# Kernel tuning notes

Measured on AMD Instinct MI355X. Metric: run time of the kernel, lower is better.

Reference implementation:

```python
import jax, jax.numpy as jnp
import numpy as np

B, T, D, U = 32, 512, 256, 1024

def setup_inputs() -> dict:
    key = jax.random.key(0)
    ks = jax.random.split(key, 5)
    return {
        "X_vecs": jax.random.normal(ks[0], (B, D), dtype=jnp.float32),
        "X_ts": jax.random.normal(ks[1], (B, T, D), dtype=jnp.float32),
        "mat_A_0": jax.random.normal(ks[2], (D, U), dtype=jnp.float32) * (1.0 / np.sqrt(D)),
        "vec_b_0": jnp.zeros((1, U), dtype=jnp.float32),
        "mat_A_s": jax.random.normal(ks[3], (D, U), dtype=jnp.float32) * (1.0 / np.sqrt(D)),
        "vec_b_s": jnp.zeros((1, U), dtype=jnp.float32),
        "mat_W_d": jax.random.normal(ks[4], (D, U), dtype=jnp.float32) * (1.0 / np.sqrt(D)),
        "vec_b_d": jnp.zeros((1, U), dtype=jnp.float32),
    }

def reference(X_vecs, X_ts, mat_A_0, vec_b_0, mat_A_s, vec_b_s, mat_W_d, vec_b_d):
    softsign = jax.nn.soft_sign  # x / (1 + |x|), the layer's main_activation
    # Learned initial state: H_0 = softsign(X_vecs @ A_0 + b_0)   [B, U]
    H0 = softsign(X_vecs @ mat_A_0 + vec_b_0)
    # Static per-step drive from the vector input (computed once, reused each t)
    drive = X_vecs @ mat_A_s + vec_b_s + vec_b_d  # [B, U]
    # Batched projection of the whole timeseries (one big GEMM instead of T small ones)
    XW = jnp.einsum('btd,du->btu', X_ts, mat_W_d)  # [B, T, U]
    def step(h, x_t):  # h: [B,U], x_t: [B,U]
        h_new = softsign(h + drive + x_t)
        return h_new, h_new
    _, outs = jax.lax.scan(step, H0, jnp.swapaxes(XW, 0, 1))  # outs: [T, B, U]
    return jnp.swapaxes(outs, 0, 1)  # return_sequences=True -> [B, T, U]
```

## Files before the change

kernel.cpp:

```cpp
#include <hip/hip_runtime.h>

#define B_DIM 32
#define T_DIM 512
#define D_DIM 256
#define U_DIM 1024
#define M_DIM (B_DIM * T_DIM)

typedef __bf16 bf16_t;
typedef bf16_t bf16x8 __attribute__((ext_vector_type(8)));
typedef float f32x4 __attribute__((ext_vector_type(4)));

__device__ __forceinline__ float ssign(float z) {
    return z * __builtin_amdgcn_rcpf(1.0f + __builtin_fabsf(z));
}

__global__ __launch_bounds__(256) void prep(const float* __restrict__ Wd,
                                            bf16_t* __restrict__ Wt,
                                            const float* __restrict__ X,
                                            bf16_t* __restrict__ Xb,
                                            const float* __restrict__ Xv,
                                            const float* __restrict__ A0,
                                            const float* __restrict__ b0,
                                            const float* __restrict__ As,
                                            const float* __restrict__ bs,
                                            const float* __restrict__ bd,
                                            float* __restrict__ H0o,
                                            float* __restrict__ Dro) {
    const int bid = blockIdx.x;
    if (bid < 64) {
        __shared__ float tile[64][65];
        const int tx = threadIdx.x & 63;
        const int ty = threadIdx.x >> 6;
        const int n0 = (bid & 15) * 64;
        const int k0 = (bid >> 4) * 64;
        #pragma unroll
        for (int rr = 0; rr < 16; ++rr) {
            const int kk = ty * 16 + rr;
            tile[kk][tx] = Wd[(size_t)(k0 + kk) * U_DIM + n0 + tx];
        }
        __syncthreads();
        #pragma unroll
        for (int rr = 0; rr < 16; ++rr) {
            const int nn = ty * 16 + rr;
            Wt[(size_t)(n0 + nn) * D_DIM + k0 + tx] = (bf16_t)tile[tx][nn];
        }
    } else if (bid < 2112) {
        const int i = ((bid - 64) * 256 + threadIdx.x) * 8;
        const float4 a = *(const float4*)(X + i);
        const float4 b = *(const float4*)(X + i + 4);
        bf16x8 p;
        p[0]=(bf16_t)a.x; p[1]=(bf16_t)a.y; p[2]=(bf16_t)a.z; p[3]=(bf16_t)a.w;
        p[4]=(bf16_t)b.x; p[5]=(bf16_t)b.y; p[6]=(bf16_t)b.z; p[7]=(bf16_t)b.w;
        *(bf16x8*)(Xb + i) = p;
    } else {
        __shared__ float xv[D_DIM];
        const int idx = bid - 2112;
        const int b = idx >> 2;
        const int u = (idx & 3) * 256 + threadIdx.x;
        xv[threadIdx.x] = Xv[(size_t)b * D_DIM + threadIdx.x];
        __syncthreads();
        float a0 = 0.f, asum = 0.f;
        #pragma unroll 8
        for (int d = 0; d < D_DIM; ++d) {
            const float x = xv[d];
            a0   = fmaf(x, A0[(size_t)d * U_DIM + u], a0);
            asum = fmaf(x, As[(size_t)d * U_DIM + u], asum);
        }
        H0o[(size_t)b * U_DIM + u] = ssign(a0 + b0[u]);
        Dro[(size_t)b * U_DIM + u] = asum + bs[u] + bd[u];
    }
}

__global__ __launch_bounds__(128, 1) void fused3(
        const float* __restrict__ H0w, const float* __restrict__ Drw,
        const bf16_t* __restrict__ Xb, const bf16_t* __restrict__ Wt,
        float* __restrict__ out) {
    __shared__ float xwT[4][64 * 20];

    const int lane = threadIdx.x & 63;
    const int wid = threadIdx.x >> 6;
    const int b = blockIdx.x;
    const int u0 = blockIdx.y * 64;

#define BARX()                                                          \
    do {                                                                \
        __asm__ volatile("s_waitcnt lgkmcnt(0)" ::: "memory");          \
        __builtin_amdgcn_s_barrier();                                   \
        __asm__ volatile("" ::: "memory");                              \
    } while (0)

    if (wid == 1) {
        const int lm = lane & 15, q = lane >> 4;
        const bf16_t* xrow = Xb + ((size_t)b * T_DIM + lm) * D_DIM + q * 8;

#define LOADA(DST, CH)                                                              \
    {                                                                               \
        const bf16_t* xp_ = xrow + (size_t)(CH) * 16 * D_DIM;                       \
        _Pragma("unroll")                                                           \
        for (int kb = 0; kb < 8; ++kb) DST[kb] = *(const bf16x8*)(xp_ + kb * 32);   \
    }

        bf16x8 af0[8], af1[8], af2[8], af3[8];
        LOADA(af0, 0); LOADA(af1, 1); LOADA(af2, 2); LOADA(af3, 3);

        bf16x8 bW[4][8];
        #pragma unroll
        for (int n = 0; n < 4; ++n)
            #pragma unroll
            for (int kb = 0; kb < 8; ++kb)
                bW[n][kb] = *(const bf16x8*)(Wt + (size_t)(u0 + n * 16 + lm) * D_DIM + kb * 32 + q * 8);

        f32x4 acc[4];
#define ZACC()                                                                      \
    {                                                                               \
        _Pragma("unroll")                                                           \
        for (int n = 0; n < 4; ++n) acc[n] = (f32x4){0.f, 0.f, 0.f, 0.f};           \
    }
#define MM(AF)                                                                      \
    {                                                                               \
        _Pragma("unroll")                                                           \
        for (int kb = 0; kb < 8; ++kb) {                                            \
            _Pragma("unroll")                                                       \
            for (int n = 0; n < 4; ++n)                                             \
                acc[n] = __builtin_amdgcn_mfma_f32_16x16x32_bf16(AF[kb], bW[n][kb], \
                                                                 acc[n], 0, 0, 0);  \
        }                                                                           \
    }
#define STASHS(SLOT)                                                                \
    {                                                                               \
        _Pragma("unroll")                                                           \
        for (int n = 0; n < 4; ++n)                                                 \
            *(f32x4*)&xwT[SLOT][(n * 16 + lm) * 20 + q * 4] = acc[n];               \
    }

        ZACC(); MM(af0); STASHS(0);
        ZACC(); MM(af1); STASHS(1);
        BARX();

        #pragma unroll 1
        for (int cc = 0; cc < 32; cc += 4) {
            if (cc + 2 < 32) { if (cc + 4 < 32) LOADA(af0, cc + 4);
                               ZACC(); MM(af2); STASHS(2); }
            BARX();
            if (cc + 3 < 32) { if (cc + 5 < 32) LOADA(af1, cc + 5);
                               ZACC(); MM(af3); STASHS(3); }
            BARX();
            if (cc + 4 < 32) { if (cc + 6 < 32) LOADA(af2, cc + 6);
                               ZACC(); MM(af0); STASHS(0); }
            BARX();
            if (cc + 5 < 32) { if (cc + 7 < 32) LOADA(af3, cc + 7);
                               ZACC(); MM(af1); STASHS(1); }
            BARX();
        }
#undef LOADA
#undef ZACC
#undef MM
#undef STASHS
    } else {
        const int u = u0 + lane;
        float h = H0w[(size_t)b * U_DIM + u];
        const float drive = Drw[(size_t)b * U_DIM + u];
        float* po = out + (size_t)b * T_DIM * U_DIM + u;

        BARX();
        const float* rb0 = &xwT[0][lane * 20];
        f32x4 v0 = *(const f32x4*)(rb0 + 0);
        f32x4 v1 = *(const f32x4*)(rb0 + 4);
        f32x4 v2 = *(const f32x4*)(rb0 + 8);
        f32x4 v3 = *(const f32x4*)(rb0 + 12);

        #pragma unroll 1
        for (int c = 0; c < 32; ++c) {
            const float* rbn = &xwT[(c + 1) & 3][lane * 20];
            f32x4 n0 = *(const f32x4*)(rbn + 0);
            f32x4 n1 = *(const f32x4*)(rbn + 4);
            f32x4 n2 = *(const f32x4*)(rbn + 8);
            f32x4 n3 = *(const f32x4*)(rbn + 12);

            float dv[16];
            #pragma unroll
            for (int r = 0; r < 4; ++r) {
                dv[r]      = drive + v0[r];
                dv[4 + r]  = drive + v1[r];
                dv[8 + r]  = drive + v2[r];
                dv[12 + r] = drive + v3[r];
            }
            #pragma unroll
            for (int j = 0; j < 16; ++j) {
                h = ssign(h + dv[j]);
                po[(size_t)(c * 16 + j) * U_DIM] = h;
            }
            BARX();
            v0 = n0; v1 = n1; v2 = n2; v3 = n3;
        }
    }
#undef BARX
}

__global__ __launch_bounds__(256) void gemm_xw_f32(const float* __restrict__ Xts,
                                                   const float* __restrict__ Wd,
                                                   float* __restrict__ out) {
    __shared__ float xs[16 * D_DIM];
    const int tid = threadIdx.x;
    const int bt0 = blockIdx.y * 16;
    const int u = blockIdx.x * 256 + tid;
    const float4* src4 = (const float4*)(Xts + (size_t)bt0 * D_DIM);
    float4* xs4 = (float4*)xs;
    #pragma unroll
    for (int i = 0; i < 4; ++i) xs4[tid + 256 * i] = src4[tid + 256 * i];
    __syncthreads();
    float acc[16];
    #pragma unroll
    for (int r = 0; r < 16; ++r) acc[r] = 0.0f;
    const float* wp = Wd + u;
    for (int d0 = 0; d0 < D_DIM; d0 += 4) {
        const float w0 = wp[(size_t)(d0 + 0) * U_DIM];
        const float w1 = wp[(size_t)(d0 + 1) * U_DIM];
        const float w2 = wp[(size_t)(d0 + 2) * U_DIM];
        const float w3 = wp[(size_t)(d0 + 3) * U_DIM];
        #pragma unroll
        for (int r = 0; r < 16; ++r) {
            const float4 xvv = *(const float4*)&xs[r * D_DIM + d0];
            acc[r] = fmaf(xvv.x, w0, acc[r]);
            acc[r] = fmaf(xvv.y, w1, acc[r]);
            acc[r] = fmaf(xvv.z, w2, acc[r]);
            acc[r] = fmaf(xvv.w, w3, acc[r]);
        }
    }
    #pragma unroll
    for (int r = 0; r < 16; ++r)
        out[(size_t)(bt0 + r) * U_DIM + u] = acc[r];
}

__global__ __launch_bounds__(256) void scan_old(const float* __restrict__ Xv,
                                                const float* __restrict__ A0,
                                                const float* __restrict__ b0,
                                                const float* __restrict__ As,
                                                const float* __restrict__ bs,
                                                const float* __restrict__ bd,
                                                float* __restrict__ out) {
    __shared__ float xv[D_DIM];
    const int tid = threadIdx.x;
    const int b = blockIdx.y;
    const int u = blockIdx.x * 256 + tid;
    xv[tid] = Xv[(size_t)b * D_DIM + tid];
    __syncthreads();
    float a0 = 0.0f, asum = 0.0f;
    #pragma unroll 4
    for (int d = 0; d < D_DIM; ++d) {
        const float x = xv[d];
        a0   = fmaf(x, A0[(size_t)d * U_DIM + u], a0);
        asum = fmaf(x, As[(size_t)d * U_DIM + u], asum);
    }
    a0 += b0[u];
    const float drive = asum + bs[u] + bd[u];
    float h = ssign(a0);
    float* po = out + (size_t)b * T_DIM * U_DIM + u;
    float buf[8];
    #pragma unroll
    for (int i = 0; i < 8; ++i) buf[i] = po[(size_t)i * U_DIM];
    for (int t = 0; t < T_DIM; t += 8) {
        #pragma unroll
        for (int i = 0; i < 8; ++i) {
            const float x = buf[i];
            const int tn = t + i + 8;
            if (tn < T_DIM) buf[i] = po[(size_t)tn * U_DIM];
            h = ssign(h + drive + x);
            po[(size_t)(t + i) * U_DIM] = h;
        }
    }
}

extern "C" void kernel_launch(void* const* d_in, const int* in_sizes, int n_in,
                              void* d_out, int out_size, void* d_ws, size_t ws_size,
                              hipStream_t stream) {
    const float* Xv  = (const float*)d_in[0];
    const float* Xts = (const float*)d_in[1];
    const float* A0  = (const float*)d_in[2];
    const float* b0  = (const float*)d_in[3];
    const float* As  = (const float*)d_in[4];
    const float* bs  = (const float*)d_in[5];
    const float* Wd  = (const float*)d_in[6];
    const float* bd  = (const float*)d_in[7];
    float* out = (float*)d_out;

    const size_t OFF_H0 = 512u << 10;
    const size_t OFF_DR = 640u << 10;
    const size_t OFF_XB = 1u << 20;
    const size_t NEED   = 16u << 20;

    if (ws_size >= NEED) {
        bf16_t* Wt = (bf16_t*)d_ws;
        float* H0w = (float*)((char*)d_ws + OFF_H0);
        float* Drw = (float*)((char*)d_ws + OFF_DR);
        bf16_t* Xb = (bf16_t*)((char*)d_ws + OFF_XB);
        prep<<<dim3(64 + M_DIM * D_DIM / (256 * 8) + 128), dim3(256), 0, stream>>>(
            Wd, Wt, Xts, Xb, Xv, A0, b0, As, bs, bd, H0w, Drw);
        fused3<<<dim3(B_DIM, U_DIM / 64), dim3(128), 0, stream>>>(H0w, Drw, Xb, Wt, out);
    } else {
        gemm_xw_f32<<<dim3(U_DIM / 256, M_DIM / 16), dim3(256), 0, stream>>>(Xts, Wd, out);
        scan_old<<<dim3(U_DIM / 256, B_DIM), dim3(256), 0, stream>>>(Xv, A0, b0, As, bs, bd, out);
    }
}
```

Baseline: 129.5 us.

## Fold prep kernel into fused scan kernel, converting inputs to bf16 in-register

Drops the separate prep launch that converted X_ts and W_d to bf16 in workspace and computed H0 and the drive vector. The fused kernel now loads fp32 X_ts directly, converts it to bf16 in registers with a two-deep prefetch, and builds W_d fragments with strided fp32 loads. The scan wave computes H0 and the drive itself. This removes one launch and the workspace round-trip, at the cost of reading twice the bytes for X_ts, every block redoing the W_d and A_0/A_s loads with uncoalesced strided access, and more register pressure.

```diff
diff --git a/kernel.cpp b/kernel.cpp
--- a/kernel.cpp
+++ b/kernel.cpp
@@ -4,7 +4,6 @@
 #define T_DIM 512
 #define D_DIM 256
 #define U_DIM 1024
-#define M_DIM (B_DIM * T_DIM)
 
 typedef __bf16 bf16_t;
 typedef bf16_t bf16x8 __attribute__((ext_vector_type(8)));
@@ -14,68 +13,14 @@
     return z * __builtin_amdgcn_rcpf(1.0f + __builtin_fabsf(z));
 }
 
-__global__ __launch_bounds__(256) void prep(const float* __restrict__ Wd,
-                                            bf16_t* __restrict__ Wt,
-                                            const float* __restrict__ X,
-                                            bf16_t* __restrict__ Xb,
-                                            const float* __restrict__ Xv,
-                                            const float* __restrict__ A0,
-                                            const float* __restrict__ b0,
-                                            const float* __restrict__ As,
-                                            const float* __restrict__ bs,
-                                            const float* __restrict__ bd,
-                                            float* __restrict__ H0o,
-                                            float* __restrict__ Dro) {
-    const int bid = blockIdx.x;
-    if (bid < 64) {
-        __shared__ float tile[64][65];
-        const int tx = threadIdx.x & 63;
-        const int ty = threadIdx.x >> 6;
-        const int n0 = (bid & 15) * 64;
-        const int k0 = (bid >> 4) * 64;
-        #pragma unroll
-        for (int rr = 0; rr < 16; ++rr) {
-            const int kk = ty * 16 + rr;
-            tile[kk][tx] = Wd[(size_t)(k0 + kk) * U_DIM + n0 + tx];
-        }
-        __syncthreads();
-        #pragma unroll
-        for (int rr = 0; rr < 16; ++rr) {
-            const int nn = ty * 16 + rr;
-            Wt[(size_t)(n0 + nn) * D_DIM + k0 + tx] = (bf16_t)tile[tx][nn];
-        }
-    } else if (bid < 2112) {
-        const int i = ((bid - 64) * 256 + threadIdx.x) * 8;
-        const float4 a = *(const float4*)(X + i);
-        const float4 b = *(const float4*)(X + i + 4);
-        bf16x8 p;
-        p[0]=(bf16_t)a.x; p[1]=(bf16_t)a.y; p[2]=(bf16_t)a.z; p[3]=(bf16_t)a.w;
-        p[4]=(bf16_t)b.x; p[5]=(bf16_t)b.y; p[6]=(bf16_t)b.z; p[7]=(bf16_t)b.w;
-        *(bf16x8*)(Xb + i) = p;
-    } else {
-        __shared__ float xv[D_DIM];
-        const int idx = bid - 2112;
-        const int b = idx >> 2;
-        const int u = (idx & 3) * 256 + threadIdx.x;
-        xv[threadIdx.x] = Xv[(size_t)b * D_DIM + threadIdx.x];
-        __syncthreads();
-        float a0 = 0.f, asum = 0.f;
-        #pragma unroll 8
-        for (int d = 0; d < D_DIM; ++d) {
-            const float x = xv[d];
-            a0   = fmaf(x, A0[(size_t)d * U_DIM + u], a0);
-            asum = fmaf(x, As[(size_t)d * U_DIM + u], asum);
-        }
-        H0o[(size_t)b * U_DIM + u] = ssign(a0 + b0[u]);
-        Dro[(size_t)b * U_DIM + u] = asum + bs[u] + bd[u];
-    }
-}
-
-__global__ __launch_bounds__(128, 1) void fused3(
-        const float* __restrict__ H0w, const float* __restrict__ Drw,
-        const bf16_t* __restrict__ Xb, const bf16_t* __restrict__ Wt,
+__global__ __launch_bounds__(128, 1) void fusedall(
+        const float* __restrict__ Xv, const float* __restrict__ Xts,
+        const float* __restrict__ A0, const float* __restrict__ b0,
+        const float* __restrict__ As, const float* __restrict__ bs,
+        const float* __restrict__ Wd, const float* __restrict__ bd,
         float* __restrict__ out) {
     __shared__ float xwT[4][64 * 20];
+    __shared__ float xvs[D_DIM];
 
     const int lane = threadIdx.x & 63;
     const int wid = threadIdx.x >> 6;
@@ -91,24 +36,51 @@
 
     if (wid == 1) {
         const int lm = lane & 15, q = lane >> 4;
-        const bf16_t* xrow = Xb + ((size_t)b * T_DIM + lm) * D_DIM + q * 8;
-
-#define LOADA(DST, CH)                                                              \
-    {                                                                               \
-        const bf16_t* xp_ = xrow + (size_t)(CH) * 16 * D_DIM;                       \
-        _Pragma("unroll")                                                           \
-        for (int kb = 0; kb < 8; ++kb) DST[kb] = *(const bf16x8*)(xp_ + kb * 32);   \
-    }
-
-        bf16x8 af0[8], af1[8], af2[8], af3[8];
-        LOADA(af0, 0); LOADA(af1, 1); LOADA(af2, 2); LOADA(af3, 3);
+        const float* xrowf = Xts + ((size_t)b * T_DIM + lm) * D_DIM + q * 8;
+
+#define LOADF(FF, CH)                                                               \
+    {                                                                               \
+        const float* xp_ = xrowf + (size_t)(CH) * 16 * D_DIM;                       \
+        _Pragma("unroll")                                                           \
+        for (int t4 = 0; t4 < 16; ++t4)                                             \
+            FF[t4] = *(const f32x4*)(xp_ + (t4 >> 1) * 32 + (t4 & 1) * 4);          \
+    }
+#define CVT(AF, FF)                                                                 \
+    {                                                                               \
+        _Pragma("unroll")                                                           \
+        for (int kb = 0; kb < 8; ++kb) {                                            \
+            bf16x8 t_;                                                              \
+            _Pragma("unroll")                                                       \
+            for (int j = 0; j < 4; ++j) {                                           \
+                t_[j]     = (bf16_t)FF[kb * 2][j];                                  \
+                t_[4 + j] = (bf16_t)FF[kb * 2 + 1][j];                              \
+            }                                                                       \
+            AF[kb] = t_;                                                            \
+        }                                                                           \
+    }
+
+        f32x4 ff0[16], ff1[16];
+        LOADF(ff0, 0);
+        LOADF(ff1, 1);
 
         bf16x8 bW[4][8];
         #pragma unroll
-        for (int n = 0; n < 4; ++n)
+        for (int n = 0; n < 4; ++n) {
             #pragma unroll
-            for (int kb = 0; kb < 8; ++kb)
-                bW[n][kb] = *(const bf16x8*)(Wt + (size_t)(u0 + n * 16 + lm) * D_DIM + kb * 32 + q * 8);
+            for (int kb = 0; kb < 8; ++kb) {
+                const float* wp = Wd + (size_t)(kb * 32 + q * 8) * U_DIM + u0 + n * 16 + lm;
+                bf16x8 t_;
+                #pragma unroll
+                for (int j = 0; j < 8; ++j) t_[j] = (bf16_t)wp[(size_t)j * U_DIM];
+                bW[n][kb] = t_;
+            }
+        }
+
+        bf16x8 afA[8], afB[8];
+        CVT(afA, ff0);
+        LOADF(ff0, 2);
+        CVT(afB, ff1);
+        LOADF(ff1, 3);
 
         f32x4 acc[4];
 #define ZACC()                                                                      \
@@ -133,33 +105,54 @@
             *(f32x4*)&xwT[SLOT][(n * 16 + lm) * 20 + q * 4] = acc[n];               \
     }
 
-        ZACC(); MM(af0); STASHS(0);
-        ZACC(); MM(af1); STASHS(1);
+        ZACC(); MM(afA); STASHS(0);
+        CVT(afA, ff0); LOADF(ff0, 4);
+        ZACC(); MM(afB); STASHS(1);
+        CVT(afB, ff1); LOADF(ff1, 5);
         BARX();
 
         #pragma unroll 1
         for (int cc = 0; cc < 32; cc += 4) {
-            if (cc + 2 < 32) { if (cc + 4 < 32) LOADA(af0, cc + 4);
-                               ZACC(); MM(af2); STASHS(2); }
-            BARX();
-            if (cc + 3 < 32) { if (cc + 5 < 32) LOADA(af1, cc + 5);
-                               ZACC(); MM(af3); STASHS(3); }
-            BARX();
-            if (cc + 4 < 32) { if (cc + 6 < 32) LOADA(af2, cc + 6);
-                               ZACC(); MM(af0); STASHS(0); }
-            BARX();
-            if (cc + 5 < 32) { if (cc + 7 < 32) LOADA(af3, cc + 7);
-                               ZACC(); MM(af1); STASHS(1); }
-            BARX();
-        }
-#undef LOADA
+            {
+                ZACC(); MM(afA); STASHS(2);
+                if (cc + 4 < 32) { CVT(afA, ff0); LOADF(ff0, ((cc + 6 < 32) ? cc + 6 : 31)); }
+            }
+            BARX();
+            {
+                ZACC(); MM(afB); STASHS(3);
+                if (cc + 5 < 32) { CVT(afB, ff1); LOADF(ff1, ((cc + 7 < 32) ? cc + 7 : 31)); }
+            }
+            BARX();
+            if (cc + 4 < 32) {
+                ZACC(); MM(afA); STASHS(0);
+                if (cc + 6 < 32) { CVT(afA, ff0); LOADF(ff0, ((cc + 8 < 32) ? cc + 8 : 31)); }
+            }
+            BARX();
+            if (cc + 5 < 32) {
+                ZACC(); MM(afB); STASHS(1);
+                if (cc + 7 < 32) { CVT(afB, ff1); LOADF(ff1, ((cc + 9 < 32) ? cc + 9 : 31)); }
+            }
+            BARX();
+        }
+#undef LOADF
+#undef CVT
 #undef ZACC
 #undef MM
 #undef STASHS
     } else {
         const int u = u0 + lane;
-        float h = H0w[(size_t)b * U_DIM + u];
-        const float drive = Drw[(size_t)b * U_DIM + u];
+
+        ((float4*)xvs)[lane] = ((const float4*)(Xv + (size_t)b * D_DIM))[lane];
+        __asm__ volatile("s_waitcnt lgkmcnt(0)" ::: "memory");
+        float a0 = 0.f, asum = 0.f;
+        #pragma unroll 16
+        for (int d = 0; d < D_DIM; ++d) {
+            const float x = xvs[d];
+            a0   = fmaf(x, A0[(size_t)d * U_DIM + u], a0);
+            asum = fmaf(x, As[(size_t)d * U_DIM + u], asum);
+        }
+        float h = ssign(a0 + b0[u]);
+        const float drive = asum + bs[u] + bd[u];
         float* po = out + (size_t)b * T_DIM * U_DIM + u;
 
         BARX();
@@ -195,80 +188,6 @@
         }
     }
 #undef BARX
-}
-
-__global__ __launch_bounds__(256) void gemm_xw_f32(const float* __restrict__ Xts,
-                                                   const float* __restrict__ Wd,
-                                                   float* __restrict__ out) {
-    __shared__ float xs[16 * D_DIM];
-    const int tid = threadIdx.x;
-    const int bt0 = blockIdx.y * 16;
-    const int u = blockIdx.x * 256 + tid;
-    const float4* src4 = (const float4*)(Xts + (size_t)bt0 * D_DIM);
-    float4* xs4 = (float4*)xs;
-    #pragma unroll
-    for (int i = 0; i < 4; ++i) xs4[tid + 256 * i] = src4[tid + 256 * i];
-    __syncthreads();
-    float acc[16];
-    #pragma unroll
-    for (int r = 0; r < 16; ++r) acc[r] = 0.0f;
-    const float* wp = Wd + u;
-    for (int d0 = 0; d0 < D_DIM; d0 += 4) {
-        const float w0 = wp[(size_t)(d0 + 0) * U_DIM];
-        const float w1 = wp[(size_t)(d0 + 1) * U_DIM];
-        const float w2 = wp[(size_t)(d0 + 2) * U_DIM];
-        const float w3 = wp[(size_t)(d0 + 3) * U_DIM];
-        #pragma unroll
-        for (int r = 0; r < 16; ++r) {
-            const float4 xvv = *(const float4*)&xs[r * D_DIM + d0];
-            acc[r] = fmaf(xvv.x, w0, acc[r]);
-            acc[r] = fmaf(xvv.y, w1, acc[r]);
-            acc[r] = fmaf(xvv.z, w2, acc[r]);
-            acc[r] = fmaf(xvv.w, w3, acc[r]);
-        }
-    }
-    #pragma unroll
-    for (int r = 0; r < 16; ++r)
-        out[(size_t)(bt0 + r) * U_DIM + u] = acc[r];
-}
-
-__global__ __launch_bounds__(256) void scan_old(const float* __restrict__ Xv,
-                                                const float* __restrict__ A0,
-                                                const float* __restrict__ b0,
-                                                const float* __restrict__ As,
-                                                const float* __restrict__ bs,
-                                                const float* __restrict__ bd,
-                                                float* __restrict__ out) {
-    __shared__ float xv[D_DIM];
-    const int tid = threadIdx.x;
-    const int b = blockIdx.y;
-    const int u = blockIdx.x * 256 + tid;
-    xv[tid] = Xv[(size_t)b * D_DIM + tid];
-    __syncthreads();
-    float a0 = 0.0f, asum = 0.0f;
-    #pragma unroll 4
-    for (int d = 0; d < D_DIM; ++d) {
-        const float x = xv[d];
-        a0   = fmaf(x, A0[(size_t)d * U_DIM + u], a0);
-        asum = fmaf(x, As[(size_t)d * U_DIM + u], asum);
-    }
-    a0 += b0[u];
-    const float drive = asum + bs[u] + bd[u];
-    float h = ssign(a0);
-    float* po = out + (size_t)b * T_DIM * U_DIM + u;
-    float buf[8];
-    #pragma unroll
-    for (int i = 0; i < 8; ++i) buf[i] = po[(size_t)i * U_DIM];
-    for (int t = 0; t < T_DIM; t += 8) {
-        #pragma unroll
-        for (int i = 0; i < 8; ++i) {
-            const float x = buf[i];
-            const int tn = t + i + 8;
-            if (tn < T_DIM) buf[i] = po[(size_t)tn * U_DIM];
-            h = ssign(h + drive + x);
-            po[(size_t)(t + i) * U_DIM] = h;
-        }
-    }
 }
 
 extern "C" void kernel_launch(void* const* d_in, const int* in_sizes, int n_in,
@@ -284,21 +203,8 @@
     const float* bd  = (const float*)d_in[7];
     float* out = (float*)d_out;
 
-    const size_t OFF_H0 = 512u << 10;
-    const size_t OFF_DR = 640u << 10;
-    const size_t OFF_XB = 1u << 20;
-    const size_t NEED   = 16u << 20;
-
-    if (ws_size >= NEED) {
-        bf16_t* Wt = (bf16_t*)d_ws;
-        float* H0w = (float*)((char*)d_ws + OFF_H0);
-        float* Drw = (float*)((char*)d_ws + OFF_DR);
-        bf16_t* Xb = (bf16_t*)((char*)d_ws + OFF_XB);
-        prep<<<dim3(64 + M_DIM * D_DIM / (256 * 8) + 128), dim3(256), 0, stream>>>(
-            Wd, Wt, Xts, Xb, Xv, A0, b0, As, bs, bd, H0w, Drw);
-        fused3<<<dim3(B_DIM, U_DIM / 64), dim3(128), 0, stream>>>(H0w, Drw, Xb, Wt, out);
-    } else {
-        gemm_xw_f32<<<dim3(U_DIM / 256, M_DIM / 16), dim3(256), 0, stream>>>(Xts, Wd, out);
-        scan_old<<<dim3(U_DIM / 256, B_DIM), dim3(256), 0, stream>>>(Xv, A0, b0, As, bs, bd, out);
-    }
+    (void)d_ws; (void)ws_size;
+
+    fusedall<<<dim3(B_DIM, U_DIM / 64), dim3(128), 0, stream>>>(
+        Xv, Xts, A0, b0, As, bs, Wd, bd, out);
 }
```

After: 149.2 us. +15.2%, slower.

## Use projective softsign recurrence and halve producer/consumer barrier count

Applied to the files above, without the earlier changes.

The scan consumer now keeps the state as a numerator/denominator pair (p, q), so each step is an fma plus an add and the reciprocal is off the serial dependency chain. The pair is renormalised every 16 steps to bound growth. The producer wave now fills two LDS slots per barrier phase, and the consumer handles 32 timesteps per barrier, which halves the number of synchronisations. This shortens the latency-bound recurrence chain but changes rounding slightly and relies on q staying finite within a 16-step window.

```diff
diff --git a/kernel.cpp b/kernel.cpp
--- a/kernel.cpp
+++ b/kernel.cpp
@@ -71,7 +71,7 @@
     }
 }
 
-__global__ __launch_bounds__(128, 1) void fused3(
+__global__ __launch_bounds__(128, 1) void fused4(
         const float* __restrict__ H0w, const float* __restrict__ Drw,
         const bf16_t* __restrict__ Xb, const bf16_t* __restrict__ Wt,
         float* __restrict__ out) {
@@ -133,23 +133,20 @@
             *(f32x4*)&xwT[SLOT][(n * 16 + lm) * 20 + q * 4] = acc[n];               \
     }
 
-        ZACC(); MM(af0); STASHS(0);
-        ZACC(); MM(af1); STASHS(1);
+        ZACC(); MM(af0); LOADA(af0, 4); STASHS(0);
+        ZACC(); MM(af1); LOADA(af1, 5); STASHS(1);
         BARX();
+        ZACC(); MM(af2); LOADA(af2, 6); STASHS(2);
+        ZACC(); MM(af3); LOADA(af3, 7); STASHS(3);
+        BARX();
 
         #pragma unroll 1
-        for (int cc = 0; cc < 32; cc += 4) {
-            if (cc + 2 < 32) { if (cc + 4 < 32) LOADA(af0, cc + 4);
-                               ZACC(); MM(af2); STASHS(2); }
+        for (int cc = 4; cc < 32; cc += 4) {
+            ZACC(); MM(af0); if (cc + 4 < 32) LOADA(af0, cc + 4); STASHS(0);
+            ZACC(); MM(af1); if (cc + 5 < 32) LOADA(af1, cc + 5); STASHS(1);
             BARX();
-            if (cc + 3 < 32) { if (cc + 5 < 32) LOADA(af1, cc + 5);
-                               ZACC(); MM(af3); STASHS(3); }
-            BARX();
-            if (cc + 4 < 32) { if (cc + 6 < 32) LOADA(af2, cc + 6);
-                               ZACC(); MM(af0); STASHS(0); }
-            BARX();
-            if (cc + 5 < 32) { if (cc + 7 < 32) LOADA(af3, cc + 7);
-                               ZACC(); MM(af1); STASHS(1); }
+            ZACC(); MM(af2); if (cc + 6 < 32) LOADA(af2, cc + 6); STASHS(2);
+            ZACC(); MM(af3); if (cc + 7 < 32) LOADA(af3, cc + 7); STASHS(3);
             BARX();
         }
 #undef LOADA
@@ -158,40 +155,47 @@
 #undef STASHS
     } else {
         const int u = u0 + lane;
-        float h = H0w[(size_t)b * U_DIM + u];
+        float pch = H0w[(size_t)b * U_DIM + u];
+        float qch = 1.0f;
         const float drive = Drw[(size_t)b * U_DIM + u];
         float* po = out + (size_t)b * T_DIM * U_DIM + u;
 
-        BARX();
-        const float* rb0 = &xwT[0][lane * 20];
-        f32x4 v0 = *(const f32x4*)(rb0 + 0);
-        f32x4 v1 = *(const f32x4*)(rb0 + 4);
-        f32x4 v2 = *(const f32x4*)(rb0 + 8);
-        f32x4 v3 = *(const f32x4*)(rb0 + 12);
-
         #pragma unroll 1
-        for (int c = 0; c < 32; ++c) {
-            const float* rbn = &xwT[(c + 1) & 3][lane * 20];
-            f32x4 n0 = *(const f32x4*)(rbn + 0);
-            f32x4 n1 = *(const f32x4*)(rbn + 4);
-            f32x4 n2 = *(const f32x4*)(rbn + 8);
-            f32x4 n3 = *(const f32x4*)(rbn + 12);
-
-            float dv[16];
+        for (int k = 0; k < 16; ++k) {
+            BARX();
+            const int s0 = (k & 1) << 1;
+            const float* r0 = &xwT[s0][lane * 20];
+            const float* r1 = &xwT[s0 + 1][lane * 20];
+            const f32x4 v0 = *(const f32x4*)(r0 + 0);
+            const f32x4 v1 = *(const f32x4*)(r0 + 4);
+            const f32x4 v2 = *(const f32x4*)(r0 + 8);
+            const f32x4 v3 = *(const f32x4*)(r0 + 12);
+            const f32x4 w0 = *(const f32x4*)(r1 + 0);
+            const f32x4 w1 = *(const f32x4*)(r1 + 4);
+            const f32x4 w2 = *(const f32x4*)(r1 + 8);
+            const f32x4 w3 = *(const f32x4*)(r1 + 12);
+
+            float dv[32];
             #pragma unroll
             for (int r = 0; r < 4; ++r) {
                 dv[r]      = drive + v0[r];
                 dv[4 + r]  = drive + v1[r];
                 dv[8 + r]  = drive + v2[r];
                 dv[12 + r] = drive + v3[r];
+                dv[16 + r] = drive + w0[r];
+                dv[20 + r] = drive + w1[r];
+                dv[24 + r] = drive + w2[r];
+                dv[28 + r] = drive + w3[r];
             }
             #pragma unroll
-            for (int j = 0; j < 16; ++j) {
-                h = ssign(h + dv[j]);
-                po[(size_t)(c * 16 + j) * U_DIM] = h;
+            for (int j = 0; j < 32; ++j) {
+                pch = fmaf(dv[j], qch, pch);
+                qch = qch + __builtin_fabsf(pch);
+                const float hh = pch * __builtin_amdgcn_rcpf(qch);
+                po[(size_t)j * U_DIM] = hh;
+                if (j == 15 || j == 31) { pch = hh; qch = 1.0f; }
             }
-            BARX();
-            v0 = n0; v1 = n1; v2 = n2; v3 = n3;
+            po += (size_t)32 * U_DIM;
         }
     }
 #undef BARX
@@ -296,7 +300,7 @@
         bf16_t* Xb = (bf16_t*)((char*)d_ws + OFF_XB);
         prep<<<dim3(64 + M_DIM * D_DIM / (256 * 8) + 128), dim3(256), 0, stream>>>(
             Wd, Wt, Xts, Xb, Xv, A0, b0, As, bs, bd, H0w, Drw);
-        fused3<<<dim3(B_DIM, U_DIM / 64), dim3(128), 0, stream>>>(H0w, Drw, Xb, Wt, out);
+        fused4<<<dim3(B_DIM, U_DIM / 64), dim3(128), 0, stream>>>(H0w, Drw, Xb, Wt, out);
     } else {
         gemm_xw_f32<<<dim3(U_DIM / 256, M_DIM / 16), dim3(256), 0, stream>>>(Xts, Wd, out);
         scan_old<<<dim3(U_DIM / 256, B_DIM), dim3(256), 0, stream>>>(Xv, A0, b0, As, bs, bd, out);
```

Result: no change. 130.1 us (+0.5%).
